# Performance work log

Measured on AMD Instinct MI355X. Metric: run time of the kernel, lower is better.

The kernel has to match this reference:

```python
import jax, jax.numpy as jnp
import numpy as np

H, E, NI = 100000, 200000, 1000000
D_H, D_E, D_OUT = 128, 64, 128
LN_EPS = 1e-5


def _linear(x, W, b):
    # torch nn.Linear convention: W is [out, in]
    return x @ W.T + b


def _scatter_mean(vals, idx, num_segments):
    # scatter_mean with empty segments producing 0 (sum=0 / max(count,1))
    s = jax.ops.segment_sum(vals, idx, num_segments=num_segments)
    c = jax.ops.segment_sum(jnp.ones((vals.shape[0], 1), vals.dtype), idx,
                            num_segments=num_segments)
    return s / jnp.maximum(c, 1.0)


def setup_inputs() -> dict:
    key = jax.random.key(0)
    ks = jax.random.split(key, 16)
    inv = lambda n: 1.0 / np.sqrt(n)
    return {
        "x_h": jax.random.normal(ks[0], (H, D_H), jnp.float32),
        "h2_edge_attr": jax.random.normal(ks[1], (E, D_E), jnp.float32),
        "Wp": jax.random.uniform(ks[2], (D_OUT, D_H), jnp.float32, -inv(D_H), inv(D_H)),
        "bp": jnp.zeros((D_OUT,), jnp.float32),
        "We1": jax.random.uniform(ks[3], (D_OUT, D_H + D_E), jnp.float32, -inv(D_H + D_E), inv(D_H + D_E)),
        "be1": jnp.zeros((D_OUT,), jnp.float32),
        "We2": jax.random.uniform(ks[4], (D_OUT, D_OUT), jnp.float32, -inv(D_OUT), inv(D_OUT)),
        "be2": jnp.zeros((D_OUT,), jnp.float32),
        "Wn1": jax.random.uniform(ks[5], (D_OUT, D_OUT), jnp.float32, -inv(D_OUT), inv(D_OUT)),
        "bn1": jnp.zeros((D_OUT,), jnp.float32),
        "Wn2": jax.random.uniform(ks[6], (D_OUT, D_OUT), jnp.float32, -inv(D_OUT), inv(D_OUT)),
        "bn2": jnp.zeros((D_OUT,), jnp.float32),
        "gamma": jnp.ones((D_OUT,), jnp.float32),
        "beta": jnp.zeros((D_OUT,), jnp.float32),
        "fg_id": jax.random.randint(ks[7], (NI,), 0, H, jnp.int32),
        "res_id": jax.random.randint(ks[8], (NI,), 0, E, jnp.int32),
    }


def reference(x_h, h2_edge_attr, Wp, bp, We1, be1, We2, be2,
              Wn1, bn1, Wn2, bn2, gamma, beta, fg_id, res_id):
    # node -> edge: mean of member node features per hyperedge
    edge_node_mean = _scatter_mean(x_h[fg_id], res_id, E)            # [E, d_h]
    e_in = jnp.concatenate([edge_node_mean, h2_edge_attr], axis=-1)  # [E, d_h+d_e]
    edge_msg = _linear(jax.nn.relu(_linear(e_in, We1, be1)), We2, be2)  # [E, d_out]
    # edge -> node: mean of incident edge messages per hypernode
    node_msg = _scatter_mean(edge_msg[res_id], fg_id, H)             # [H, d_out]
    z = _linear(x_h, Wp, bp) + _linear(jax.nn.relu(_linear(node_msg, Wn1, bn1)), Wn2, bn2)
    z = jax.nn.relu(z)
    mu = jnp.mean(z, axis=-1, keepdims=True)
    var = jnp.var(z, axis=-1, keepdims=True)
    return (z - mu) * jax.lax.rsqrt(var + LN_EPS) * gamma + beta
```

## Files before the change

kernel.cpp:

```cpp
#include <hip/hip_runtime.h>

#define H_N   100000
#define E_N   200000
#define NI_N  1000000
#define LN_EPS 1e-5f

#define NBUCK  1563
#define SEGB_E 128
#define SEGB_H 64
#define CAP    1024
#define SUBCAP 192

typedef __attribute__((ext_vector_type(8))) short bf16x8;
typedef __attribute__((ext_vector_type(4))) float floatx4;

__device__ inline unsigned short f2bf(float f) {
  unsigned u = __builtin_bit_cast(unsigned, f);
  u += 0x7fffu + ((u >> 16) & 1u);
  return (unsigned short)(u >> 16);
}
__device__ inline float bf2f(unsigned short s) {
  unsigned u = ((unsigned)s) << 16;
  return __builtin_bit_cast(float, u);
}
__device__ inline unsigned get_xcc() {
  unsigned x;
  asm volatile("s_getreg_b32 %0, hwreg(HW_REG_XCC_ID)" : "=s"(x));
  return x & 7;
}

__global__ __launch_bounds__(256) void k_cvt_bf16(const float4* __restrict__ src,
                                                  unsigned short* __restrict__ dst,
                                                  int n4) {
  int i = blockIdx.x * 256 + threadIdx.x;
  if (i >= n4) return;
  float4 v = src[i];
  union { unsigned short us[4]; unsigned long long u64; } p;
  p.us[0] = f2bf(v.x); p.us[1] = f2bf(v.y);
  p.us[2] = f2bf(v.z); p.us[3] = f2bf(v.w);
  *(unsigned long long*)(dst + (size_t)i * 4) = p.u64;
}

__global__ __launch_bounds__(256) void k_bucket(
    const int* __restrict__ fg, const int* __restrict__ res,
    int* __restrict__ bcnt_e, int* __restrict__ bcnt_h,
    unsigned* __restrict__ pairs_e, unsigned* __restrict__ pairs_h) {
  int i = blockIdx.x * 256 + threadIdx.x;
  if (i >= NI_N) return;
  unsigned xcc = get_xcc();
  int f = fg[i], r = res[i];
  int be = r >> 7, se = r & 127;
  int pe = atomicAdd(bcnt_e + xcc * NBUCK + be, 1);
  if (pe < SUBCAP)
    pairs_e[((size_t)xcc * NBUCK + be) * SUBCAP + pe] =
        ((unsigned)se << 24) | (unsigned)f;
  int bh = f >> 6, sh = f & 63;
  int ph = atomicAdd(bcnt_h + xcc * NBUCK + bh, 1);
  if (ph < SUBCAP)
    pairs_h[((size_t)xcc * NBUCK + bh) * SUBCAP + ph] =
        ((unsigned)sh << 24) | (unsigned)r;
}

__global__ __launch_bounds__(256) void k_seg_mean(
    const unsigned short* __restrict__ rows, const unsigned* __restrict__ pairs,
    const int* __restrict__ bcnt, unsigned short* __restrict__ outm,
    int nseg, int segb) {
  __shared__ unsigned raw[CAP];
  __shared__ unsigned sortedp[CAP];
  __shared__ int cnts[129];
  __shared__ int curs[128];
  const int b = blockIdx.x;
  const int t = threadIdx.x;

  int total = 0;
#pragma unroll
  for (int x = 0; x < 8; ++x) {
    int c = min(bcnt[x * NBUCK + b], SUBCAP);
    const unsigned* src = pairs + ((size_t)x * NBUCK + b) * SUBCAP;
    for (int j = t; j < c; j += 256) {
      int d = total + j;
      if (d < CAP) raw[d] = src[j];
    }
    total += c;
  }
  const int cnt = min(total, CAP);
  if (t <= segb) cnts[t] = 0;
  __syncthreads();
  for (int j = t; j < cnt; j += 256)
    atomicAdd(&cnts[(raw[j] >> 24) + 1], 1);
  __syncthreads();
  for (int d = 1; d <= segb; d <<= 1) {
    int v = 0;
    if (t <= segb && t >= d) v = cnts[t - d];
    __syncthreads();
    if (t <= segb) cnts[t] += v;
    __syncthreads();
  }
  if (t < segb) curs[t] = cnts[t];
  __syncthreads();
  for (int j = t; j < cnt; j += 256) {
    unsigned p = raw[j];
    int s = p >> 24;
    int d = atomicAdd(&curs[s], 1);
    sortedp[d] = p & 0xFFFFFFu;
  }
  __syncthreads();

  const int wave = t >> 6, lane = t & 63;
  const int segs_here = min(segb, nseg - b * segb);
  for (int s = wave; s < segs_here; s += 4) {
    int o = cnts[s], e = cnts[s + 1];
    float a0 = 0.f, a1 = 0.f;
    int j = o;
    for (; j + 1 < e; j += 2) {
      int i0 = sortedp[j], i1 = sortedp[j + 1];
      unsigned v0 = *(const unsigned*)(rows + (size_t)i0 * 128 + lane * 2);
      unsigned v1 = *(const unsigned*)(rows + (size_t)i1 * 128 + lane * 2);
      a0 += bf2f((unsigned short)(v0 & 0xffffu)) + bf2f((unsigned short)(v1 & 0xffffu));
      a1 += bf2f((unsigned short)(v0 >> 16)) + bf2f((unsigned short)(v1 >> 16));
    }
    if (j < e) {
      int i0 = sortedp[j];
      unsigned v0 = *(const unsigned*)(rows + (size_t)i0 * 128 + lane * 2);
      a0 += bf2f((unsigned short)(v0 & 0xffffu));
      a1 += bf2f((unsigned short)(v0 >> 16));
    }
    float inv = (e > o) ? 1.0f / (float)(e - o) : 0.0f;
    unsigned ov = (unsigned)f2bf(a0 * inv) | ((unsigned)f2bf(a1 * inv) << 16);
    *(unsigned*)(outm + (size_t)(b * segb + s) * 128 + lane * 2) = ov;
  }
}

__global__ __launch_bounds__(256, 4) void k_edge_mlp(
    const short* __restrict__ edge_mean, const short* __restrict__ attr_bf,
    const short* __restrict__ w1, const float* __restrict__ b1,
    const short* __restrict__ w2, const float* __restrict__ b2,
    unsigned short* __restrict__ edge_msg) {
  __shared__ short h1s[64][136];
  const int wave = threadIdx.x >> 6;
  const int lane = threadIdx.x & 63;
  const int row  = lane & 15;
  const int quad = lane >> 4;
  const int e0   = blockIdx.x * 64;
  const int cb   = wave * 32;

  bf16x8 B1[2][6];
#pragma unroll
  for (int nl = 0; nl < 2; ++nl)
#pragma unroll
    for (int ks = 0; ks < 6; ++ks)
      B1[nl][ks] = *(const bf16x8*)(w1 + (size_t)(cb + nl * 16 + row) * 192 +
                                    ks * 32 + quad * 8);

  floatx4 acc[4][2];
#pragma unroll
  for (int m = 0; m < 4; ++m)
#pragma unroll
    for (int nl = 0; nl < 2; ++nl) acc[m][nl] = (floatx4){0.f, 0.f, 0.f, 0.f};

#pragma unroll
  for (int ks = 0; ks < 6; ++ks) {
    bf16x8 a[4];
#pragma unroll
    for (int m = 0; m < 4; ++m) {
      int e = e0 + m * 16 + row;
      if (ks < 4) {
        a[m] = *(const bf16x8*)(edge_mean + (size_t)e * 128 + ks * 32 + quad * 8);
      } else {
        a[m] = *(const bf16x8*)(attr_bf + (size_t)e * 64 + (ks - 4) * 32 + quad * 8);
      }
    }
#pragma unroll
    for (int m = 0; m < 4; ++m)
#pragma unroll
      for (int nl = 0; nl < 2; ++nl)
        acc[m][nl] = __builtin_amdgcn_mfma_f32_16x16x32_bf16(a[m], B1[nl][ks],
                                                             acc[m][nl], 0, 0, 0);
  }

#pragma unroll
  for (int nl = 0; nl < 2; ++nl) {
    float bias = b1[cb + nl * 16 + row];
#pragma unroll
    for (int m = 0; m < 4; ++m)
#pragma unroll
      for (int r = 0; r < 4; ++r)
        h1s[m * 16 + quad * 4 + r][cb + nl * 16 + row] =
            (short)f2bf(fmaxf(acc[m][nl][r] + bias, 0.0f));
  }

  bf16x8 B2[2][4];
#pragma unroll
  for (int nl = 0; nl < 2; ++nl)
#pragma unroll
    for (int ks = 0; ks < 4; ++ks)
      B2[nl][ks] = *(const bf16x8*)(w2 + (size_t)(cb + nl * 16 + row) * 128 +
                                    ks * 32 + quad * 8);
  __syncthreads();

  floatx4 acc2[4][2];
#pragma unroll
  for (int m = 0; m < 4; ++m)
#pragma unroll
    for (int nl = 0; nl < 2; ++nl) acc2[m][nl] = (floatx4){0.f, 0.f, 0.f, 0.f};

#pragma unroll
  for (int ks = 0; ks < 4; ++ks) {
    bf16x8 a[4];
#pragma unroll
    for (int m = 0; m < 4; ++m)
      a[m] = *(const bf16x8*)&h1s[m * 16 + row][ks * 32 + quad * 8];
#pragma unroll
    for (int m = 0; m < 4; ++m)
#pragma unroll
      for (int nl = 0; nl < 2; ++nl)
        acc2[m][nl] = __builtin_amdgcn_mfma_f32_16x16x32_bf16(a[m], B2[nl][ks],
                                                              acc2[m][nl], 0, 0, 0);
  }

#pragma unroll
  for (int nl = 0; nl < 2; ++nl) {
    int col = cb + nl * 16 + row;
    float bias = b2[col];
#pragma unroll
    for (int m = 0; m < 4; ++m)
#pragma unroll
      for (int r = 0; r < 4; ++r)
        edge_msg[(size_t)(e0 + m * 16 + quad * 4 + r) * 128 + col] =
            f2bf(acc2[m][nl][r] + bias);
  }
}

__global__ __launch_bounds__(256, 3) void k_node_mlp_ln(
    const short* __restrict__ node_msg, const short* __restrict__ xh_bf,
    const short* __restrict__ wp, const float* __restrict__ bp,
    const short* __restrict__ wn1, const float* __restrict__ bn1,
    const short* __restrict__ wn2, const float* __restrict__ bn2,
    const float* __restrict__ gamma, const float* __restrict__ beta,
    float* __restrict__ out) {
  __shared__ short h1s[64][136];
  __shared__ float2 part[64][4];
  const int wave = threadIdx.x >> 6;
  const int lane = threadIdx.x & 63;
  const int row  = lane & 15;
  const int quad = lane >> 4;
  const int n0   = blockIdx.x * 64;
  const int cb   = wave * 32;

  bf16x8 B1[2][4];
#pragma unroll
  for (int nl = 0; nl < 2; ++nl)
#pragma unroll
    for (int ks = 0; ks < 4; ++ks)
      B1[nl][ks] = *(const bf16x8*)(wn1 + (size_t)(cb + nl * 16 + row) * 128 +
                                    ks * 32 + quad * 8);

  floatx4 acc[4][2];
#pragma unroll
  for (int m = 0; m < 4; ++m)
#pragma unroll
    for (int nl = 0; nl < 2; ++nl) acc[m][nl] = (floatx4){0.f, 0.f, 0.f, 0.f};

#pragma unroll
  for (int ks = 0; ks < 4; ++ks) {
    bf16x8 a[4];
#pragma unroll
    for (int m = 0; m < 4; ++m) {
      int n = n0 + m * 16 + row;
      a[m] = *(const bf16x8*)(node_msg + (size_t)n * 128 + ks * 32 + quad * 8);
    }
#pragma unroll
    for (int m = 0; m < 4; ++m)
#pragma unroll
      for (int nl = 0; nl < 2; ++nl)
        acc[m][nl] = __builtin_amdgcn_mfma_f32_16x16x32_bf16(a[m], B1[nl][ks],
                                                             acc[m][nl], 0, 0, 0);
  }

#pragma unroll
  for (int nl = 0; nl < 2; ++nl) {
    float bias = bn1[cb + nl * 16 + row];
#pragma unroll
    for (int m = 0; m < 4; ++m)
#pragma unroll
      for (int r = 0; r < 4; ++r)
        h1s[m * 16 + quad * 4 + r][cb + nl * 16 + row] =
            (short)f2bf(fmaxf(acc[m][nl][r] + bias, 0.0f));
  }

  bf16x8 B2[2][4], Bp[2][4];
#pragma unroll
  for (int nl = 0; nl < 2; ++nl)
#pragma unroll
    for (int ks = 0; ks < 4; ++ks) {
      B2[nl][ks] = *(const bf16x8*)(wn2 + (size_t)(cb + nl * 16 + row) * 128 +
                                    ks * 32 + quad * 8);
      Bp[nl][ks] = *(const bf16x8*)(wp + (size_t)(cb + nl * 16 + row) * 128 +
                                    ks * 32 + quad * 8);
    }
  __syncthreads();

  floatx4 acc2[4][2];
#pragma unroll
  for (int m = 0; m < 4; ++m)
#pragma unroll
    for (int nl = 0; nl < 2; ++nl) acc2[m][nl] = (floatx4){0.f, 0.f, 0.f, 0.f};

#pragma unroll
  for (int ks = 0; ks < 4; ++ks) {
    bf16x8 at[4], ax[4];
#pragma unroll
    for (int m = 0; m < 4; ++m) {
      at[m] = *(const bf16x8*)&h1s[m * 16 + row][ks * 32 + quad * 8];
      int n = n0 + m * 16 + row;
      ax[m] = *(const bf16x8*)(xh_bf + (size_t)n * 128 + ks * 32 + quad * 8);
    }
#pragma unroll
    for (int m = 0; m < 4; ++m)
#pragma unroll
      for (int nl = 0; nl < 2; ++nl) {
        acc2[m][nl] = __builtin_amdgcn_mfma_f32_16x16x32_bf16(at[m], B2[nl][ks],
                                                              acc2[m][nl], 0, 0, 0);
        acc2[m][nl] = __builtin_amdgcn_mfma_f32_16x16x32_bf16(ax[m], Bp[nl][ks],
                                                              acc2[m][nl], 0, 0, 0);
      }
  }

  float z[4][2][4];
#pragma unroll
  for (int m = 0; m < 4; ++m) {
    float s[4], ss[4];
#pragma unroll
    for (int r = 0; r < 4; ++r) { s[r] = 0.f; ss[r] = 0.f; }
#pragma unroll
    for (int nl = 0; nl < 2; ++nl) {
      float bias = bp[cb + nl * 16 + row] + bn2[cb + nl * 16 + row];
#pragma unroll
      for (int r = 0; r < 4; ++r) {
        float v = fmaxf(acc2[m][nl][r] + bias, 0.0f);
        z[m][nl][r] = v;
        s[r] += v;
        ss[r] += v * v;
      }
    }
#pragma unroll
    for (int r = 0; r < 4; ++r) {
#pragma unroll
      for (int msk = 1; msk < 16; msk <<= 1) {
        s[r]  += __shfl_xor(s[r],  msk, 64);
        ss[r] += __shfl_xor(ss[r], msk, 64);
      }
      if (row == 0) part[m * 16 + quad * 4 + r][wave] = make_float2(s[r], ss[r]);
    }
  }
  __syncthreads();

#pragma unroll
  for (int m = 0; m < 4; ++m)
#pragma unroll
    for (int r = 0; r < 4; ++r) {
      int rr = m * 16 + quad * 4 + r;
      float2 p0 = part[rr][0], p1 = part[rr][1], p2 = part[rr][2], p3 = part[rr][3];
      float mean = (p0.x + p1.x + p2.x + p3.x) * (1.0f / 128.0f);
      float var  = (p0.y + p1.y + p2.y + p3.y) * (1.0f / 128.0f) - mean * mean;
      float rstd = rsqrtf(var + LN_EPS);
      int n = n0 + rr;
      if (n < H_N) {
#pragma unroll
        for (int nl = 0; nl < 2; ++nl) {
          int col = cb + nl * 16 + row;
          out[(size_t)n * 128 + col] =
              (z[m][nl][r] - mean) * rstd * gamma[col] + beta[col];
        }
      }
    }
}

extern "C" void kernel_launch(void* const* d_in, const int* in_sizes, int n_in,
                              void* d_out, int out_size, void* d_ws, size_t ws_size,
                              hipStream_t stream) {
  const float* x_h   = (const float*)d_in[0];
  const float* attr  = (const float*)d_in[1];
  const float* Wp    = (const float*)d_in[2];
  const float* bp    = (const float*)d_in[3];
  const float* We1   = (const float*)d_in[4];
  const float* be1   = (const float*)d_in[5];
  const float* We2   = (const float*)d_in[6];
  const float* be2   = (const float*)d_in[7];
  const float* Wn1   = (const float*)d_in[8];
  const float* bn1   = (const float*)d_in[9];
  const float* Wn2   = (const float*)d_in[10];
  const float* bn2   = (const float*)d_in[11];
  const float* gamma = (const float*)d_in[12];
  const float* beta  = (const float*)d_in[13];
  const int*   fg    = (const int*)d_in[14];
  const int*   res   = (const int*)d_in[15];
  float* out = (float*)d_out;

  int* bcnt_e = (int*)d_ws;
  int* bcnt_h = bcnt_e + 8 * NBUCK;
  unsigned* pairs_e = (unsigned*)(bcnt_h + 8 * NBUCK);
  unsigned* pairs_h = pairs_e + (size_t)8 * NBUCK * SUBCAP;
  unsigned short* xh_bf     = (unsigned short*)(pairs_h + (size_t)8 * NBUCK * SUBCAP);
  unsigned short* edge_mean = xh_bf + (size_t)H_N * 128;
  unsigned short* edge_msg  = edge_mean + (size_t)E_N * 128;
  unsigned short* node_msg  = edge_msg + (size_t)E_N * 128;
  short* w1  = (short*)(node_msg + (size_t)H_N * 128);
  short* w2  = w1 + 128 * 192;
  short* wn1 = w2 + 128 * 128;
  short* wn2 = wn1 + 128 * 128;
  short* wp  = wn2 + 128 * 128;
  short* attr_bf = wp + 128 * 128;

  hipMemsetAsync(bcnt_e, 0, (size_t)16 * NBUCK * 4, stream);

  {
    int n4 = H_N * 128 / 4;
    k_cvt_bf16<<<(n4 + 255) / 256, 256, 0, stream>>>((const float4*)x_h, xh_bf, n4);
    n4 = E_N * 64 / 4;
    k_cvt_bf16<<<(n4 + 255) / 256, 256, 0, stream>>>((const float4*)attr, (unsigned short*)attr_bf, n4);
    n4 = 128 * 192 / 4;
    k_cvt_bf16<<<(n4 + 255) / 256, 256, 0, stream>>>((const float4*)We1, (unsigned short*)w1, n4);
    n4 = 128 * 128 / 4;
    k_cvt_bf16<<<(n4 + 255) / 256, 256, 0, stream>>>((const float4*)We2, (unsigned short*)w2, n4);
    k_cvt_bf16<<<(n4 + 255) / 256, 256, 0, stream>>>((const float4*)Wn1, (unsigned short*)wn1, n4);
    k_cvt_bf16<<<(n4 + 255) / 256, 256, 0, stream>>>((const float4*)Wn2, (unsigned short*)wn2, n4);
    k_cvt_bf16<<<(n4 + 255) / 256, 256, 0, stream>>>((const float4*)Wp, (unsigned short*)wp, n4);
  }

  k_bucket<<<(NI_N + 255) / 256, 256, 0, stream>>>(fg, res, bcnt_e, bcnt_h,
                                                   pairs_e, pairs_h);

  k_seg_mean<<<NBUCK, 256, 0, stream>>>(xh_bf, pairs_e, bcnt_e,
                                        edge_mean, E_N, SEGB_E);
  k_edge_mlp<<<E_N / 64, 256, 0, stream>>>((const short*)edge_mean, attr_bf,
                                           w1, be1, w2, be2, edge_msg);
  k_seg_mean<<<NBUCK, 256, 0, stream>>>(edge_msg, pairs_h, bcnt_h,
                                        node_msg, H_N, SEGB_H);
  k_node_mlp_ln<<<(H_N + 63) / 64, 256, 0, stream>>>((const short*)node_msg,
                                                     (const short*)xh_bf,
                                                     wp, bp, wn1, bn1, wn2, bn2,
                                                     gamma, beta, out);
}
```

Before: 520.9 us.

## Fuse segment-mean gathers into edge and node MLP kernels via LDS

Merges the scatter-mean kernels into the following MLP kernels. Each block gathers and averages its 64 segments into shared memory and feeds the MFMA directly from there, which drops the edge_mean and node_msg round trips through global memory and two launches. Edge buckets shrink to 64 segments each so they line up with the 64-row MLP tile. The bucketing kernel now handles 4 indices per thread with vector nontemporal loads, and its counters are padded to separate cache lines to reduce atomic contention. The cost is that gather latency and MLP compute now share one block, and shared memory is reused across both phases, which may lower occupancy.

```diff
diff --git a/kernel.cpp b/kernel.cpp
--- a/kernel.cpp
+++ b/kernel.cpp
@@ -5,14 +5,17 @@
 #define NI_N  1000000
 #define LN_EPS 1e-5f
 
-#define NBUCK  1563
-#define SEGB_E 128
-#define SEGB_H 64
-#define CAP    1024
-#define SUBCAP 192
+#define NBUCK_E 3125
+#define NBUCK_H 1563
+#define SUBCAP_E 128
+#define SUBCAP_H 192
+#define CAP_E 512
+#define CAP_H 1024
+#define BCNT_PAD 16
 
 typedef __attribute__((ext_vector_type(8))) short bf16x8;
 typedef __attribute__((ext_vector_type(4))) float floatx4;
+typedef __attribute__((ext_vector_type(4))) int intx4;
 
 __device__ inline unsigned short f2bf(float f) {
   unsigned u = __builtin_bit_cast(unsigned, f);
@@ -45,103 +48,104 @@
     const int* __restrict__ fg, const int* __restrict__ res,
     int* __restrict__ bcnt_e, int* __restrict__ bcnt_h,
     unsigned* __restrict__ pairs_e, unsigned* __restrict__ pairs_h) {
-  int i = blockIdx.x * 256 + threadIdx.x;
-  if (i >= NI_N) return;
+  int i0 = (blockIdx.x * 256 + threadIdx.x) * 4;
+  if (i0 >= NI_N) return;
   unsigned xcc = get_xcc();
-  int f = fg[i], r = res[i];
-  int be = r >> 7, se = r & 127;
-  int pe = atomicAdd(bcnt_e + xcc * NBUCK + be, 1);
-  if (pe < SUBCAP)
-    pairs_e[((size_t)xcc * NBUCK + be) * SUBCAP + pe] =
-        ((unsigned)se << 24) | (unsigned)f;
-  int bh = f >> 6, sh = f & 63;
-  int ph = atomicAdd(bcnt_h + xcc * NBUCK + bh, 1);
-  if (ph < SUBCAP)
-    pairs_h[((size_t)xcc * NBUCK + bh) * SUBCAP + ph] =
-        ((unsigned)sh << 24) | (unsigned)r;
-}
-
-__global__ __launch_bounds__(256) void k_seg_mean(
-    const unsigned short* __restrict__ rows, const unsigned* __restrict__ pairs,
-    const int* __restrict__ bcnt, unsigned short* __restrict__ outm,
-    int nseg, int segb) {
-  __shared__ unsigned raw[CAP];
-  __shared__ unsigned sortedp[CAP];
-  __shared__ int cnts[129];
-  __shared__ int curs[128];
+  intx4 f4 = __builtin_nontemporal_load((const intx4*)(fg + i0));
+  intx4 r4 = __builtin_nontemporal_load((const intx4*)(res + i0));
+#pragma unroll
+  for (int j = 0; j < 4; ++j) {
+    int f = f4[j], r = r4[j];
+    int be = r >> 6, se = r & 63;
+    int pe = atomicAdd(bcnt_e + ((size_t)xcc * NBUCK_E + be) * BCNT_PAD, 1);
+    if (pe < SUBCAP_E)
+      pairs_e[((size_t)xcc * NBUCK_E + be) * SUBCAP_E + pe] =
+          ((unsigned)se << 24) | (unsigned)f;
+    int bh = f >> 6, sh = f & 63;
+    int ph = atomicAdd(bcnt_h + ((size_t)xcc * NBUCK_H + bh) * BCNT_PAD, 1);
+    if (ph < SUBCAP_H)
+      pairs_h[((size_t)xcc * NBUCK_H + bh) * SUBCAP_H + ph] =
+          ((unsigned)sh << 24) | (unsigned)r;
+  }
+}
+
+__global__ __launch_bounds__(256, 4) void k_edge_fused(
+    const unsigned short* __restrict__ xh, const short* __restrict__ attr_bf,
+    const unsigned* __restrict__ pairs, const int* __restrict__ bcnt,
+    const short* __restrict__ w1, const float* __restrict__ b1,
+    const short* __restrict__ w2, const float* __restrict__ b2,
+    unsigned short* __restrict__ edge_msg) {
+  __shared__ short meanS[64][136];
+  __shared__ int ubuf[4352];
+  short (*h1s)[136] = (short(*)[136])ubuf;
+  unsigned* raw = (unsigned*)ubuf;
+  unsigned* sortedp = raw + CAP_E;
+  int* cnts = (int*)(sortedp + CAP_E);
+  int* curs = cnts + 65;
+
   const int b = blockIdx.x;
   const int t = threadIdx.x;
 
   int total = 0;
 #pragma unroll
   for (int x = 0; x < 8; ++x) {
-    int c = min(bcnt[x * NBUCK + b], SUBCAP);
-    const unsigned* src = pairs + ((size_t)x * NBUCK + b) * SUBCAP;
+    int c = min(bcnt[((size_t)x * NBUCK_E + b) * BCNT_PAD], SUBCAP_E);
+    const unsigned* src = pairs + ((size_t)x * NBUCK_E + b) * SUBCAP_E;
     for (int j = t; j < c; j += 256) {
       int d = total + j;
-      if (d < CAP) raw[d] = src[j];
+      if (d < CAP_E) raw[d] = src[j];
     }
     total += c;
   }
-  const int cnt = min(total, CAP);
-  if (t <= segb) cnts[t] = 0;
+  const int cnt = min(total, CAP_E);
+  if (t <= 64) cnts[t] = 0;
   __syncthreads();
   for (int j = t; j < cnt; j += 256)
     atomicAdd(&cnts[(raw[j] >> 24) + 1], 1);
   __syncthreads();
-  for (int d = 1; d <= segb; d <<= 1) {
+  for (int d = 1; d <= 64; d <<= 1) {
     int v = 0;
-    if (t <= segb && t >= d) v = cnts[t - d];
+    if (t <= 64 && t >= d) v = cnts[t - d];
     __syncthreads();
-    if (t <= segb) cnts[t] += v;
+    if (t <= 64) cnts[t] += v;
     __syncthreads();
   }
-  if (t < segb) curs[t] = cnts[t];
+  if (t < 64) curs[t] = cnts[t];
   __syncthreads();
   for (int j = t; j < cnt; j += 256) {
     unsigned p = raw[j];
-    int s = p >> 24;
-    int d = atomicAdd(&curs[s], 1);
+    int d = atomicAdd(&curs[p >> 24], 1);
     sortedp[d] = p & 0xFFFFFFu;
   }
   __syncthreads();
 
   const int wave = t >> 6, lane = t & 63;
-  const int segs_here = min(segb, nseg - b * segb);
-  for (int s = wave; s < segs_here; s += 4) {
+  for (int s = wave; s < 64; s += 4) {
     int o = cnts[s], e = cnts[s + 1];
     float a0 = 0.f, a1 = 0.f;
     int j = o;
     for (; j + 1 < e; j += 2) {
       int i0 = sortedp[j], i1 = sortedp[j + 1];
-      unsigned v0 = *(const unsigned*)(rows + (size_t)i0 * 128 + lane * 2);
-      unsigned v1 = *(const unsigned*)(rows + (size_t)i1 * 128 + lane * 2);
+      unsigned v0 = *(const unsigned*)(xh + (size_t)i0 * 128 + lane * 2);
+      unsigned v1 = *(const unsigned*)(xh + (size_t)i1 * 128 + lane * 2);
       a0 += bf2f((unsigned short)(v0 & 0xffffu)) + bf2f((unsigned short)(v1 & 0xffffu));
       a1 += bf2f((unsigned short)(v0 >> 16)) + bf2f((unsigned short)(v1 >> 16));
     }
     if (j < e) {
       int i0 = sortedp[j];
-      unsigned v0 = *(const unsigned*)(rows + (size_t)i0 * 128 + lane * 2);
+      unsigned v0 = *(const unsigned*)(xh + (size_t)i0 * 128 + lane * 2);
       a0 += bf2f((unsigned short)(v0 & 0xffffu));
       a1 += bf2f((unsigned short)(v0 >> 16));
     }
     float inv = (e > o) ? 1.0f / (float)(e - o) : 0.0f;
-    unsigned ov = (unsigned)f2bf(a0 * inv) | ((unsigned)f2bf(a1 * inv) << 16);
-    *(unsigned*)(outm + (size_t)(b * segb + s) * 128 + lane * 2) = ov;
-  }
-}
-
-__global__ __launch_bounds__(256, 4) void k_edge_mlp(
-    const short* __restrict__ edge_mean, const short* __restrict__ attr_bf,
-    const short* __restrict__ w1, const float* __restrict__ b1,
-    const short* __restrict__ w2, const float* __restrict__ b2,
-    unsigned short* __restrict__ edge_msg) {
-  __shared__ short h1s[64][136];
-  const int wave = threadIdx.x >> 6;
-  const int lane = threadIdx.x & 63;
+    *(unsigned*)&meanS[s][lane * 2] =
+        (unsigned)f2bf(a0 * inv) | ((unsigned)f2bf(a1 * inv) << 16);
+  }
+  __syncthreads();
+
   const int row  = lane & 15;
   const int quad = lane >> 4;
-  const int e0   = blockIdx.x * 64;
+  const int e0   = b * 64;
   const int cb   = wave * 32;
 
   bf16x8 B1[2][6];
@@ -163,10 +167,10 @@
     bf16x8 a[4];
 #pragma unroll
     for (int m = 0; m < 4; ++m) {
-      int e = e0 + m * 16 + row;
       if (ks < 4) {
-        a[m] = *(const bf16x8*)(edge_mean + (size_t)e * 128 + ks * 32 + quad * 8);
+        a[m] = *(const bf16x8*)&meanS[m * 16 + row][ks * 32 + quad * 8];
       } else {
+        int e = e0 + m * 16 + row;
         a[m] = *(const bf16x8*)(attr_bf + (size_t)e * 64 + (ks - 4) * 32 + quad * 8);
       }
     }
@@ -231,20 +235,91 @@
   }
 }
 
-__global__ __launch_bounds__(256, 3) void k_node_mlp_ln(
-    const short* __restrict__ node_msg, const short* __restrict__ xh_bf,
+__global__ __launch_bounds__(256, 3) void k_node_fused(
+    const unsigned short* __restrict__ emsg, const short* __restrict__ xh_bf,
+    const unsigned* __restrict__ pairs, const int* __restrict__ bcnt,
     const short* __restrict__ wp, const float* __restrict__ bp,
     const short* __restrict__ wn1, const float* __restrict__ bn1,
     const short* __restrict__ wn2, const float* __restrict__ bn2,
     const float* __restrict__ gamma, const float* __restrict__ beta,
     float* __restrict__ out) {
-  __shared__ short h1s[64][136];
+  __shared__ short meanS[64][136];
+  __shared__ int ubuf[4352];
   __shared__ float2 part[64][4];
-  const int wave = threadIdx.x >> 6;
-  const int lane = threadIdx.x & 63;
+  short (*h1s)[136] = (short(*)[136])ubuf;
+  unsigned* raw = (unsigned*)ubuf;
+  unsigned* sortedp = raw + CAP_H;
+  int* cnts = (int*)(sortedp + CAP_H);
+  int* curs = cnts + 65;
+
+  const int b = blockIdx.x;
+  const int t = threadIdx.x;
+
+  int total = 0;
+#pragma unroll
+  for (int x = 0; x < 8; ++x) {
+    int c = min(bcnt[((size_t)x * NBUCK_H + b) * BCNT_PAD], SUBCAP_H);
+    const unsigned* src = pairs + ((size_t)x * NBUCK_H + b) * SUBCAP_H;
+    for (int j = t; j < c; j += 256) {
+      int d = total + j;
+      if (d < CAP_H) raw[d] = src[j];
+    }
+    total += c;
+  }
+  const int cnt = min(total, CAP_H);
+  if (t <= 64) cnts[t] = 0;
+  __syncthreads();
+  for (int j = t; j < cnt; j += 256)
+    atomicAdd(&cnts[(raw[j] >> 24) + 1], 1);
+  __syncthreads();
+  for (int d = 1; d <= 64; d <<= 1) {
+    int v = 0;
+    if (t <= 64 && t >= d) v = cnts[t - d];
+    __syncthreads();
+    if (t <= 64) cnts[t] += v;
+    __syncthreads();
+  }
+  if (t < 64) curs[t] = cnts[t];
+  __syncthreads();
+  for (int j = t; j < cnt; j += 256) {
+    unsigned p = raw[j];
+    int d = atomicAdd(&curs[p >> 24], 1);
+    sortedp[d] = p & 0xFFFFFFu;
+  }
+  __syncthreads();
+
+  const int wave = t >> 6, lane = t & 63;
+  const int segs_here = min(64, H_N - b * 64);
+  for (int s = wave; s < 64; s += 4) {
+    if (s < segs_here) {
+      int o = cnts[s], e = cnts[s + 1];
+      float a0 = 0.f, a1 = 0.f;
+      int j = o;
+      for (; j + 1 < e; j += 2) {
+        int i0 = sortedp[j], i1 = sortedp[j + 1];
+        unsigned v0 = *(const unsigned*)(emsg + (size_t)i0 * 128 + lane * 2);
+        unsigned v1 = *(const unsigned*)(emsg + (size_t)i1 * 128 + lane * 2);
+        a0 += bf2f((unsigned short)(v0 & 0xffffu)) + bf2f((unsigned short)(v1 & 0xffffu));
+        a1 += bf2f((unsigned short)(v0 >> 16)) + bf2f((unsigned short)(v1 >> 16));
+      }
+      if (j < e) {
+        int i0 = sortedp[j];
+        unsigned v0 = *(const unsigned*)(emsg + (size_t)i0 * 128 + lane * 2);
+        a0 += bf2f((unsigned short)(v0 & 0xffffu));
+        a1 += bf2f((unsigned short)(v0 >> 16));
+      }
+      float inv = (e > o) ? 1.0f / (float)(e - o) : 0.0f;
+      *(unsigned*)&meanS[s][lane * 2] =
+          (unsigned)f2bf(a0 * inv) | ((unsigned)f2bf(a1 * inv) << 16);
+    } else {
+      *(unsigned*)&meanS[s][lane * 2] = 0u;
+    }
+  }
+  __syncthreads();
+
   const int row  = lane & 15;
   const int quad = lane >> 4;
-  const int n0   = blockIdx.x * 64;
+  const int n0   = b * 64;
   const int cb   = wave * 32;
 
   bf16x8 B1[2][4];
@@ -265,10 +340,8 @@
   for (int ks = 0; ks < 4; ++ks) {
     bf16x8 a[4];
 #pragma unroll
-    for (int m = 0; m < 4; ++m) {
-      int n = n0 + m * 16 + row;
-      a[m] = *(const bf16x8*)(node_msg + (size_t)n * 128 + ks * 32 + quad * 8);
-    }
+    for (int m = 0; m < 4; ++m)
+      a[m] = *(const bf16x8*)&meanS[m * 16 + row][ks * 32 + quad * 8];
 #pragma unroll
     for (int m = 0; m < 4; ++m)
 #pragma unroll
@@ -398,21 +471,20 @@
   float* out = (float*)d_out;
 
   int* bcnt_e = (int*)d_ws;
-  int* bcnt_h = bcnt_e + 8 * NBUCK;
-  unsigned* pairs_e = (unsigned*)(bcnt_h + 8 * NBUCK);
-  unsigned* pairs_h = pairs_e + (size_t)8 * NBUCK * SUBCAP;
-  unsigned short* xh_bf     = (unsigned short*)(pairs_h + (size_t)8 * NBUCK * SUBCAP);
-  unsigned short* edge_mean = xh_bf + (size_t)H_N * 128;
-  unsigned short* edge_msg  = edge_mean + (size_t)E_N * 128;
-  unsigned short* node_msg  = edge_msg + (size_t)E_N * 128;
-  short* w1  = (short*)(node_msg + (size_t)H_N * 128);
+  int* bcnt_h = bcnt_e + (size_t)8 * NBUCK_E * BCNT_PAD;
+  unsigned* pairs_e = (unsigned*)(bcnt_h + (size_t)8 * NBUCK_H * BCNT_PAD);
+  unsigned* pairs_h = pairs_e + (size_t)8 * NBUCK_E * SUBCAP_E;
+  unsigned short* xh_bf    = (unsigned short*)(pairs_h + (size_t)8 * NBUCK_H * SUBCAP_H);
+  unsigned short* edge_msg = xh_bf + (size_t)H_N * 128;
+  short* w1  = (short*)(edge_msg + (size_t)E_N * 128);
   short* w2  = w1 + 128 * 192;
   short* wn1 = w2 + 128 * 128;
   short* wn2 = wn1 + 128 * 128;
   short* wp  = wn2 + 128 * 128;
   short* attr_bf = wp + 128 * 128;
 
-  hipMemsetAsync(bcnt_e, 0, (size_t)16 * NBUCK * 4, stream);
+  hipMemsetAsync(bcnt_e, 0,
+                 (size_t)(8 * NBUCK_E + 8 * NBUCK_H) * BCNT_PAD * 4, stream);
 
   {
     int n4 = H_N * 128 / 4;
@@ -428,17 +500,13 @@
     k_cvt_bf16<<<(n4 + 255) / 256, 256, 0, stream>>>((const float4*)Wp, (unsigned short*)wp, n4);
   }
 
-  k_bucket<<<(NI_N + 255) / 256, 256, 0, stream>>>(fg, res, bcnt_e, bcnt_h,
-                                                   pairs_e, pairs_h);
-
-  k_seg_mean<<<NBUCK, 256, 0, stream>>>(xh_bf, pairs_e, bcnt_e,
-                                        edge_mean, E_N, SEGB_E);
-  k_edge_mlp<<<E_N / 64, 256, 0, stream>>>((const short*)edge_mean, attr_bf,
-                                           w1, be1, w2, be2, edge_msg);
-  k_seg_mean<<<NBUCK, 256, 0, stream>>>(edge_msg, pairs_h, bcnt_h,
-                                        node_msg, H_N, SEGB_H);
-  k_node_mlp_ln<<<(H_N + 63) / 64, 256, 0, stream>>>((const short*)node_msg,
-                                                     (const short*)xh_bf,
-                                                     wp, bp, wn1, bn1, wn2, bn2,
-                                                     gamma, beta, out);
-}
+  k_bucket<<<(NI_N / 4 + 255) / 256, 256, 0, stream>>>(fg, res, bcnt_e, bcnt_h,
+                                                       pairs_e, pairs_h);
+
+  k_edge_fused<<<NBUCK_E, 256, 0, stream>>>(xh_bf, attr_bf, pairs_e, bcnt_e,
+                                            w1, be1, w2, be2, edge_msg);
+  k_node_fused<<<NBUCK_H, 256, 0, stream>>>(edge_msg, (const short*)xh_bf,
+                                            pairs_h, bcnt_h,
+                                            wp, bp, wn1, bn1, wn2, bn2,
+                                            gamma, beta, out);
+}
```

Result: no change. 529.6 us (+1.7%).
